# Performance work log

Measured on AMD Instinct MI355X. Metric: run time of the kernel, lower is better.

The kernel has to match this reference:

```python
import jax, jax.numpy as jnp
import numpy as np

H = 16  # heads
DH = 64  # dim_head
SCALE = DH ** -0.5


def rotate_half(x):
    x1, x2 = jnp.split(x, 2, axis=-1)
    return jnp.concatenate([-x2, x1], axis=-1)


def apply_rope(pos, t):
    # pos: [n, d] broadcast over [b, h, n, d]
    return t * jnp.cos(pos) + rotate_half(t) * jnp.sin(pos)


def setup_inputs() -> dict:
    key = jax.random.key(0)
    ks = jax.random.split(key, 6)
    B, N, D = 4, 2048, 1024
    inner = H * DH
    x = jax.random.normal(ks[0], (B, N, D), dtype=jnp.float32)
    rotary_emb = jax.random.normal(ks[1], (N, DH), dtype=jnp.float32)
    Wq = jax.random.normal(ks[2], (D, inner), dtype=jnp.float32) / np.sqrt(D)
    Wkv = jax.random.normal(ks[3], (D, 2 * inner), dtype=jnp.float32) / np.sqrt(D)
    Wout = jax.random.normal(ks[4], (inner, D), dtype=jnp.float32) / np.sqrt(inner)
    bout = jnp.zeros((D,), dtype=jnp.float32)
    return {"x": x, "rotary_emb": rotary_emb, "Wq": Wq, "Wkv": Wkv, "Wout": Wout, "bout": bout}


def reference(x, rotary_emb, Wq, Wkv, Wout, bout):
    B, N, D = x.shape
    # QKV projections (self-attention: context = x)
    q = x @ Wq                       # [b, n, h*d]
    kv = x @ Wkv                     # [b, n, 2*h*d]
    k, v = jnp.split(kv, 2, axis=-1)

    def to_heads(t):
        return t.reshape(B, N, H, DH).transpose(0, 2, 1, 3)  # [b, h, n, d]

    q, k, v = to_heads(q), to_heads(k), to_heads(v)
    q = apply_rope(rotary_emb, q)
    k = apply_rope(rotary_emb, k)

    # scaled dot-product attention
    scores = jnp.einsum('bhid,bhjd->bhij', q, k) * SCALE
    attn = jax.nn.softmax(scores, axis=-1)
    out = jnp.einsum('bhij,bhjd->bhid', attn, v)  # [b, h, n, d]
    out = out.transpose(0, 2, 1, 3).reshape(B, N, H * DH)
    return out @ Wout + bout
```

## Files before the change

### kernel.cpp

```cpp
#include <hip/hip_runtime.h>

#define BB 4
#define NN 2048
#define DD 1024
#define HH 16
#define DHH 64
#define MM (BB*NN)
#define QS 3072

typedef unsigned short u16;
typedef __attribute__((ext_vector_type(8))) short short8;
typedef __attribute__((ext_vector_type(4))) float floatx4;

#if __has_builtin(__builtin_amdgcn_exp2f)
#define EXP2F __builtin_amdgcn_exp2f
#else
#define EXP2F exp2f
#endif

__device__ __forceinline__ u16 f2bf(float f) {
  union { float f; unsigned u; } v; v.f = f;
  unsigned u = v.u;
  return (u16)((u + 0x7fffu + ((u >> 16) & 1u)) >> 16);
}
__device__ __forceinline__ float bf2f(u16 h) {
  union { unsigned u; float f; } v; v.u = ((unsigned)h) << 16;
  return v.f;
}
__device__ __forceinline__ unsigned fbits(float f) {
  union { float f; unsigned u; } v; v.f = f; return v.u;
}
__device__ __forceinline__ unsigned pkbf(float lo, float hi) {
#if __has_builtin(__builtin_amdgcn_perm)
  return __builtin_amdgcn_perm(fbits(hi), fbits(lo), 0x07060302u);
#else
  return (fbits(lo) >> 16) | (fbits(hi) & 0xffff0000u);
#endif
}
__device__ __forceinline__ void gll16(const u16* g, u16* l) {
  __builtin_amdgcn_global_load_lds((const __attribute__((address_space(1))) unsigned int*)g,
                                   (__attribute__((address_space(3))) unsigned int*)l, 16, 0, 0);
}
__device__ __forceinline__ int toff(int row, int kc) {
  int pr = row >> 1;
  int c = (((row & 1) << 2) + kc) ^ (pr & 7);
  return pr * 64 + c * 8;
}

#define SOFTMAX_SCALE 0.18033688f
#define SOFTMAX_BIAS  -28.8539008f

__global__ __launch_bounds__(256) void cvt_kernel(const float* __restrict__ in,
                                                  u16* __restrict__ out, int n) {
  int i = (blockIdx.x * 256 + threadIdx.x) * 4;
  if (i >= n) return;
  float4 v = *(const float4*)(in + i);
  u16 o[4] = {f2bf(v.x), f2bf(v.y), f2bf(v.z), f2bf(v.w)};
  *(uint2*)(out + i) = *(uint2*)o;
}

__global__ __launch_bounds__(256) void tcvt3_kernel(const float* __restrict__ Wq,
                                                    const float* __restrict__ Wkv,
                                                    const float* __restrict__ Wout,
                                                    u16* __restrict__ WT,
                                                    u16* __restrict__ WoutT) {
  __shared__ float t[64][65];
  int bx = blockIdx.x;
  const float* src;
  u16* dst;
  int C, c0;
  if (bx < 16)      { src = Wq;   dst = WT;                       C = 1024; c0 = bx * 64; }
  else if (bx < 48) { src = Wkv;  dst = WT + (size_t)DD * DD;     C = 2048; c0 = (bx - 16) * 64; }
  else              { src = Wout; dst = WoutT;                    C = 1024; c0 = (bx - 48) * 64; }
  const int R = 1024;
  int r0 = blockIdx.y * 64;
  int tid = threadIdx.x;
#pragma unroll
  for (int i = 0; i < 16; ++i) {
    int lin = i * 256 + tid;
    int rr = lin >> 6, cc = lin & 63;
    t[rr][cc] = src[(size_t)(r0 + rr) * C + c0 + cc];
  }
  __syncthreads();
#pragma unroll
  for (int i = 0; i < 16; ++i) {
    int lin = i * 256 + tid;
    int rr = lin >> 6, cc = lin & 63;
    dst[(size_t)(c0 + rr) * R + r0 + cc] = f2bf(t[cc][rr]);
  }
}

__global__ __launch_bounds__(256) void rope_tab_kernel(const float* __restrict__ rot,
                                                       float2* __restrict__ tab) {
  int i = blockIdx.x * 256 + threadIdx.x;
  float p = rot[i];
  float s, c;
  __sincosf(p, &s, &c);
  tab[i] = make_float2(c, s);
}

__global__ __launch_bounds__(256) void gemm_qkv(const u16* __restrict__ A,
                                                const u16* __restrict__ Bt,
                                                u16* __restrict__ qd,
                                                u16* __restrict__ kd,
                                                u16* __restrict__ vt,
                                                const float2* __restrict__ tab) {
  const int K = DD;
  __shared__ __align__(16) u16 lds[16384];
  int tid = threadIdx.x;
  int wave = tid >> 6, lane = tid & 63;
  int q4 = lane >> 4, l16 = lane & 15;
  int m0 = blockIdx.y * 128, n0 = blockIdx.x * 128;
  int wm = (wave >> 1) * 64, wn = (wave & 1) * 64;

  const u16* Ag = A + (size_t)m0 * K;
  const u16* Bg = Bt + (size_t)n0 * K;
  int o1 = tid, o2 = tid + 256;
  int pr1 = o1 >> 3, c1 = (o1 & 7) ^ (pr1 & 7);
  int row1 = pr1 * 2 + (c1 >> 2), kc1 = (c1 & 3) * 8;
  int pr2 = o2 >> 3, c2 = (o2 & 7) ^ (pr2 & 7);
  int row2 = pr2 * 2 + (c2 >> 2), kc2 = (c2 & 3) * 8;
  int d1 = wave * 512, d2 = 2048 + wave * 512;

  int foA[4], foB[4];
#pragma unroll
  for (int i = 0; i < 4; ++i) {
    foA[i] = toff(wm + i * 16 + l16, q4);
    foB[i] = toff(wn + i * 16 + l16, q4);
  }

  floatx4 acc[4][4];
#pragma unroll
  for (int mi = 0; mi < 4; ++mi)
#pragma unroll
    for (int ni = 0; ni < 4; ++ni) acc[mi][ni] = (floatx4){0.f, 0.f, 0.f, 0.f};

  gll16(Ag + (size_t)row1 * K + kc1, lds + d1);
  gll16(Ag + (size_t)row2 * K + kc2, lds + d2);
  gll16(Bg + (size_t)row1 * K + kc1, lds + 8192 + d1);
  gll16(Bg + (size_t)row2 * K + kc2, lds + 8192 + d2);

  for (int k0 = 0, it = 0; k0 < K; k0 += 32, ++it) {
    int boff = (it & 1) * 4096;
    if (k0 + 32 < K) {
      int nboff = 4096 - boff;
      int kn = k0 + 32;
      gll16(Ag + (size_t)row1 * K + kn + kc1, lds + nboff + d1);
      gll16(Ag + (size_t)row2 * K + kn + kc2, lds + nboff + d2);
      gll16(Bg + (size_t)row1 * K + kn + kc1, lds + 8192 + nboff + d1);
      gll16(Bg + (size_t)row2 * K + kn + kc2, lds + 8192 + nboff + d2);
      __builtin_amdgcn_s_waitcnt(0x0F74);
    } else {
      __builtin_amdgcn_s_waitcnt(0x0F70);
    }
    __builtin_amdgcn_s_barrier();
    const u16* Ac = lds + boff;
    const u16* Bc = lds + 8192 + boff;
    short8 af[4], bfr[4];
#pragma unroll
    for (int i = 0; i < 4; ++i) {
      af[i]  = *(const short8*)(Ac + foA[i]);
      bfr[i] = *(const short8*)(Bc + foB[i]);
    }
#pragma unroll
    for (int mi = 0; mi < 4; ++mi)
#pragma unroll
      for (int ni = 0; ni < 4; ++ni)
        acc[mi][ni] = __builtin_amdgcn_mfma_f32_16x16x32_bf16(af[mi], bfr[ni], acc[mi][ni], 0, 0, 0);
    __builtin_amdgcn_s_barrier();
  }

  int colbase = n0 + wn;
  int slot = colbase >> 10;
  int h = (colbase >> 6) & 15;
#pragma unroll
  for (int mi = 0; mi < 4; ++mi) {
    int mbase = m0 + wm + mi * 16 + q4 * 4;
    float vals[4][4];
    if (slot < 2) {
      float sc = slot ? 1.0f : SOFTMAX_SCALE;
#pragma unroll
      for (int r = 0; r < 4; ++r) {
        int n = (mbase + r) & (NN - 1);
#pragma unroll
        for (int ni = 0; ni < 2; ++ni) {
          int d0 = ni * 16 + l16;
          float2 cs0 = tab[n * 64 + d0];
          float2 cs1 = tab[n * 64 + d0 + 32];
          float v0 = acc[mi][ni][r], v1 = acc[mi][ni + 2][r];
          vals[ni][r]     = (v0 * cs0.x - v1 * cs0.y) * sc;
          vals[ni + 2][r] = (v1 * cs1.x + v0 * cs1.y) * sc;
        }
      }
      u16* dst = slot ? kd : qd;
#pragma unroll
      for (int ni = 0; ni < 4; ++ni)
#pragma unroll
        for (int r = 0; r < 4; ++r) {
          int m = mbase + r;
          dst[((size_t)((m >> 11) * HH + h) * NN + (m & (NN - 1))) * 64 + ni * 16 + l16] =
              f2bf(vals[ni][r]);
        }
    } else {
#pragma unroll
      for (int ni = 0; ni < 4; ++ni) {
        int d = ni * 16 + l16;
#pragma unroll
        for (int r = 0; r < 4; ++r) {
          int m = mbase + r;
          int nn = m & (NN - 1);
          vt[(size_t)((m >> 11) * HH + h) * (NN * 64) + (nn >> 6) * 4096 + d * 64 + (nn & 63)] =
              f2bf(acc[mi][ni][r]);
        }
      }
    }
  }
}

__global__ __launch_bounds__(256) void gemm_out(const u16* __restrict__ A,
                                                const u16* __restrict__ Bt,
                                                float* __restrict__ Cout,
                                                const float* __restrict__ bias,
                                                int M, int N, int K) {
  __shared__ __align__(16) u16 lds[16384];
  int tid = threadIdx.x;
  int wave = tid >> 6, lane = tid & 63;
  int q4 = lane >> 4, l16 = lane & 15;
  int m0 = blockIdx.y * 128, n0 = blockIdx.x * 128;
  int wm = (wave >> 1) * 64, wn = (wave & 1) * 64;

  const u16* Ag = A + (size_t)m0 * K;
  const u16* Bg = Bt + (size_t)n0 * K;
  int o1 = tid, o2 = tid + 256;
  int pr1 = o1 >> 3, c1 = (o1 & 7) ^ (pr1 & 7);
  int row1 = pr1 * 2 + (c1 >> 2), kc1 = (c1 & 3) * 8;
  int pr2 = o2 >> 3, c2 = (o2 & 7) ^ (pr2 & 7);
  int row2 = pr2 * 2 + (c2 >> 2), kc2 = (c2 & 3) * 8;
  int d1 = wave * 512, d2 = 2048 + wave * 512;

  int foA[4], foB[4];
#pragma unroll
  for (int i = 0; i < 4; ++i) {
    foA[i] = toff(wm + i * 16 + l16, q4);
    foB[i] = toff(wn + i * 16 + l16, q4);
  }

  floatx4 acc[4][4];
#pragma unroll
  for (int mi = 0; mi < 4; ++mi)
#pragma unroll
    for (int ni = 0; ni < 4; ++ni) acc[mi][ni] = (floatx4){0.f, 0.f, 0.f, 0.f};

  gll16(Ag + (size_t)row1 * K + kc1, lds + d1);
  gll16(Ag + (size_t)row2 * K + kc2, lds + d2);
  gll16(Bg + (size_t)row1 * K + kc1, lds + 8192 + d1);
  gll16(Bg + (size_t)row2 * K + kc2, lds + 8192 + d2);

  for (int k0 = 0, it = 0; k0 < K; k0 += 32, ++it) {
    int boff = (it & 1) * 4096;
    if (k0 + 32 < K) {
      int nboff = 4096 - boff;
      int kn = k0 + 32;
      gll16(Ag + (size_t)row1 * K + kn + kc1, lds + nboff + d1);
      gll16(Ag + (size_t)row2 * K + kn + kc2, lds + nboff + d2);
      gll16(Bg + (size_t)row1 * K + kn + kc1, lds + 8192 + nboff + d1);
      gll16(Bg + (size_t)row2 * K + kn + kc2, lds + 8192 + nboff + d2);
      __builtin_amdgcn_s_waitcnt(0x0F74);
    } else {
      __builtin_amdgcn_s_waitcnt(0x0F70);
    }
    __builtin_amdgcn_s_barrier();
    const u16* Ac = lds + boff;
    const u16* Bc = lds + 8192 + boff;
    short8 af[4], bfr[4];
#pragma unroll
    for (int i = 0; i < 4; ++i) {
      af[i]  = *(const short8*)(Ac + foA[i]);
      bfr[i] = *(const short8*)(Bc + foB[i]);
    }
#pragma unroll
    for (int mi = 0; mi < 4; ++mi)
#pragma unroll
      for (int ni = 0; ni < 4; ++ni)
        acc[mi][ni] = __builtin_amdgcn_mfma_f32_16x16x32_bf16(af[mi], bfr[ni], acc[mi][ni], 0, 0, 0);
    __builtin_amdgcn_s_barrier();
  }

#pragma unroll
  for (int ni = 0; ni < 4; ++ni) {
    int col = n0 + wn + ni * 16 + l16;
    float bval = bias[col];
#pragma unroll
    for (int mi = 0; mi < 4; ++mi) {
#pragma unroll
      for (int r = 0; r < 4; ++r) {
        int row = m0 + wm + mi * 16 + q4 * 4 + r;
        Cout[(size_t)row * N + col] = acc[mi][ni][r] + bval;
      }
    }
  }
}

__global__ __launch_bounds__(512, 4) void attn_kernel(const u16* __restrict__ qd,
                                                      const u16* __restrict__ kd,
                                                      const u16* __restrict__ vt,
                                                      u16* __restrict__ ao) {
  __shared__ __align__(16) u16 lds[16384];

  int tid = threadIdx.x, wave = tid >> 6, lane = tid & 63;
  int q4 = lane >> 4, l16 = lane & 15;
  int qt = blockIdx.x, bh = blockIdx.y, b = bh >> 4, h = bh & 15;
  const u16* qbh = qd + (size_t)bh * NN * 64;
  const u16* kbh = kd + (size_t)bh * NN * 64;
  const u16* vbh = vt + (size_t)bh * NN * 64;

  int srow = wave * 8 + (lane >> 3);
  int g = ((lane & 7) ^ ((lane >> 3) & 7)) * 8;
  int prow = ((srow >> 2) & 3) * 8 + ((srow >> 4) & 1) * 4 + (srow & 3) + ((srow >> 5) & 1) * 32;

#pragma unroll
  for (int it = 0; it < 4; ++it)
    gll16(qbh + (size_t)(qt * 256 + it * 64 + srow) * 64 + g, lds + (it * 64 + wave * 8) * 64);
  __builtin_amdgcn_s_waitcnt(0x0F70);
  __builtin_amdgcn_s_barrier();

  short8 aq[2][2];
#pragma unroll
  for (int mi = 0; mi < 2; ++mi)
#pragma unroll
    for (int ks = 0; ks < 2; ++ks) {
      int row = wave * 32 + mi * 16 + l16;
      aq[mi][ks] = *(const short8*)(lds + row * 64 + (((ks * 4 + q4) ^ (row & 7)) * 8));
    }
  __builtin_amdgcn_s_waitcnt(0xC07F);
  __builtin_amdgcn_s_barrier();

  gll16(kbh + (size_t)prow * 64 + g, lds + wave * 512);
  gll16(vbh + (size_t)srow * 64 + g, lds + 8192 + wave * 512);

  union { unsigned u[4]; short8 s8; } ones;
#pragma unroll
  for (int i = 0; i < 4; ++i) ones.u[i] = 0x3F803F80u;

  floatx4 lacc[2];
  floatx4 o[2][4];
#pragma unroll
  for (int mi = 0; mi < 2; ++mi) {
    lacc[mi] = (floatx4){0.f, 0.f, 0.f, 0.f};
#pragma unroll
    for (int di = 0; di < 4; ++di) o[mi][di] = (floatx4){0.f, 0.f, 0.f, 0.f};
  }

  for (int j0 = 0, itn = 0; j0 < NN; j0 += 64, ++itn) {
    int coff = (itn & 1) * 4096;
    if (j0 + 64 < NN) {
      int noff = 4096 - coff;
      gll16(kbh + (size_t)(j0 + 64 + prow) * 64 + g, lds + noff + wave * 512);
      gll16(vbh + (size_t)((j0 >> 6) + 1) * 4096 + srow * 64 + g, lds + 8192 + noff + wave * 512);
      __builtin_amdgcn_s_waitcnt(0x0F72);
    } else {
      __builtin_amdgcn_s_waitcnt(0x0F70);
    }
    __builtin_amdgcn_s_barrier();

    const u16* Kc = lds + coff;
    const u16* Vc = lds + 8192 + coff;

    floatx4 s[4][2];
#pragma unroll
    for (int kg = 0; kg < 4; ++kg)
#pragma unroll
      for (int mi = 0; mi < 2; ++mi)
        s[kg][mi] = (floatx4){SOFTMAX_BIAS, SOFTMAX_BIAS, SOFTMAX_BIAS, SOFTMAX_BIAS};
#pragma unroll
    for (int ks = 0; ks < 2; ++ks) {
      short8 kf[4];
#pragma unroll
      for (int kg = 0; kg < 4; ++kg) {
        int row = kg * 16 + l16;
        kf[kg] = *(const short8*)(Kc + row * 64 + (((ks * 4 + q4) ^ (row & 7)) * 8));
      }
#pragma unroll
      for (int kg = 0; kg < 4; ++kg)
#pragma unroll
        for (int mi = 0; mi < 2; ++mi)
          s[kg][mi] = __builtin_amdgcn_mfma_f32_16x16x32_bf16(kf[kg], aq[mi][ks], s[kg][mi], 0, 0, 0);
    }

    unsigned pk[4][2][2];
#pragma unroll
    for (int kg = 0; kg < 4; ++kg)
#pragma unroll
      for (int mi = 0; mi < 2; ++mi) {
        float e0 = EXP2F(s[kg][mi][0]);
        float e1 = EXP2F(s[kg][mi][1]);
        float e2 = EXP2F(s[kg][mi][2]);
        float e3 = EXP2F(s[kg][mi][3]);
        pk[kg][mi][0] = pkbf(e0, e1);
        pk[kg][mi][1] = pkbf(e2, e3);
      }

#pragma unroll
    for (int ks = 0; ks < 2; ++ks) {
      short8 vf[4];
#pragma unroll
      for (int di = 0; di < 4; ++di) {
        int row = di * 16 + l16;
        vf[di] = *(const short8*)(Vc + row * 64 + (((ks * 4 + q4) ^ (row & 7)) * 8));
      }
#pragma unroll
      for (int mi = 0; mi < 2; ++mi) {
        union { unsigned u[4]; short8 s8; } bw;
        bw.u[0] = pk[2 * ks][mi][0];
        bw.u[1] = pk[2 * ks][mi][1];
        bw.u[2] = pk[2 * ks + 1][mi][0];
        bw.u[3] = pk[2 * ks + 1][mi][1];
        lacc[mi] = __builtin_amdgcn_mfma_f32_16x16x32_bf16(ones.s8, bw.s8, lacc[mi], 0, 0, 0);
#pragma unroll
        for (int di = 0; di < 4; ++di)
          o[mi][di] = __builtin_amdgcn_mfma_f32_16x16x32_bf16(vf[di], bw.s8, o[mi][di], 0, 0, 0);
      }
    }
    __builtin_amdgcn_s_barrier();
  }

  float rinv[2];
#pragma unroll
  for (int mi = 0; mi < 2; ++mi) rinv[mi] = 1.0f / lacc[mi][0];

#pragma unroll
  for (int mi = 0; mi < 2; ++mi) {
    int qrow = qt * 256 + wave * 32 + mi * 16 + l16;
    size_t base = (size_t)(b * NN + qrow) * DD + h * DHH + q4 * 4;
#pragma unroll
    for (int di = 0; di < 4; ++di)
#pragma unroll
      for (int r = 0; r < 4; ++r)
        ao[base + di * 16 + r] = f2bf(o[mi][di][r] * rinv[mi]);
  }
}

extern "C" void kernel_launch(void* const* d_in, const int* in_sizes, int n_in,
                              void* d_out, int out_size, void* d_ws, size_t ws_size,
                              hipStream_t stream) {
  const float* x    = (const float*)d_in[0];
  const float* rot  = (const float*)d_in[1];
  const float* Wq   = (const float*)d_in[2];
  const float* Wkv  = (const float*)d_in[3];
  const float* Wout = (const float*)d_in[4];
  const float* bout = (const float*)d_in[5];
  float* out = (float*)d_out;

  char* ws = (char*)d_ws;
  size_t off = 0;
  auto alloc = [&](size_t bytes) {
    void* p = ws + off;
    off = (off + bytes + 255) & ~(size_t)255;
    return p;
  };
  u16*    xb    = (u16*)alloc((size_t)MM * DD * 2);
  u16*    WT    = (u16*)alloc((size_t)QS * DD * 2);
  u16*    WoutT = (u16*)alloc((size_t)DD * DD * 2);
  float2* tab   = (float2*)alloc((size_t)NN * DHH * 8);
  u16*    qdb   = (u16*)alloc((size_t)MM * DD * 2);
  u16*    kdb   = (u16*)alloc((size_t)MM * DD * 2);
  u16*    vtt   = (u16*)alloc((size_t)MM * DD * 2);
  u16*    ao    = (u16*)alloc((size_t)MM * DD * 2);

  cvt_kernel<<<(MM * DD / 4) / 256, 256, 0, stream>>>(x, xb, MM * DD);
  tcvt3_kernel<<<dim3(64, 16), 256, 0, stream>>>(Wq, Wkv, Wout, WT, WoutT);
  rope_tab_kernel<<<(NN * DHH) / 256, 256, 0, stream>>>(rot, tab);

  gemm_qkv<<<dim3(QS / 128, MM / 128), 256, 0, stream>>>(xb, WT, qdb, kdb, vtt, tab);

  attn_kernel<<<dim3(NN / 256, BB * HH), 512, 0, stream>>>(qdb, kdb, vtt, ao);

  gemm_out<<<dim3(DD / 128, MM / 128), 256, 0, stream>>>(ao, WoutT, out, bout, MM, DD, DD);
}
```

Measured before the change: 270.8 us.

## Restructure QKV GEMM into 256x256 tiles with staged half-tile prefetch pipeline

The QKV projection GEMM moves from 128x128 tiles on 4 waves to 256x256 tiles on 8 waves with K-steps of 64. Global-to-LDS loads are split into half-tile stages interleaved between MFMA phases, with s_setprio around the MFMA blocks. Workgroup indices are remapped so that neighbouring blocks share input tiles in cache. The aim is more data reuse per LDS byte and better overlap of loads with compute, at the cost of 128 KB of LDS and heavy register pressure from 32 accumulators, which can limit occupancy.

```diff
diff --git a/kernel.cpp b/kernel.cpp
--- a/kernel.cpp
+++ b/kernel.cpp
@@ -99,86 +99,136 @@
   tab[i] = make_float2(c, s);
 }
 
-__global__ __launch_bounds__(256) void gemm_qkv(const u16* __restrict__ A,
-                                                const u16* __restrict__ Bt,
-                                                u16* __restrict__ qd,
-                                                u16* __restrict__ kd,
-                                                u16* __restrict__ vt,
-                                                const float2* __restrict__ tab) {
+__global__ __launch_bounds__(512, 2) void gemm_qkv(const u16* __restrict__ A,
+                                                   const u16* __restrict__ Bt,
+                                                   u16* __restrict__ qd,
+                                                   u16* __restrict__ kd,
+                                                   u16* __restrict__ vt,
+                                                   const float2* __restrict__ tab) {
   const int K = DD;
-  __shared__ __align__(16) u16 lds[16384];
+  const int NT = K / 64;
+  __shared__ __align__(16) u16 lds[65536];
   int tid = threadIdx.x;
   int wave = tid >> 6, lane = tid & 63;
   int q4 = lane >> 4, l16 = lane & 15;
-  int m0 = blockIdx.y * 128, n0 = blockIdx.x * 128;
-  int wm = (wave >> 1) * 64, wn = (wave & 1) * 64;
+  int wr = wave >> 2, wc = wave & 3;
+
+  int flat = blockIdx.y * 12 + blockIdx.x;
+  int wg = (flat & 7) * 48 + (flat >> 3);
+  int bx = wg % 12, by = wg / 12;
+  int m0 = by * 256, n0 = bx * 256;
 
   const u16* Ag = A + (size_t)m0 * K;
   const u16* Bg = Bt + (size_t)n0 * K;
-  int o1 = tid, o2 = tid + 256;
-  int pr1 = o1 >> 3, c1 = (o1 & 7) ^ (pr1 & 7);
-  int row1 = pr1 * 2 + (c1 >> 2), kc1 = (c1 & 3) * 8;
-  int pr2 = o2 >> 3, c2 = (o2 & 7) ^ (pr2 & 7);
-  int row2 = pr2 * 2 + (c2 >> 2), kc2 = (c2 & 3) * 8;
-  int d1 = wave * 512, d2 = 2048 + wave * 512;
-
-  int foA[4], foB[4];
-#pragma unroll
-  for (int i = 0; i < 4; ++i) {
-    foA[i] = toff(wm + i * 16 + l16, q4);
-    foB[i] = toff(wn + i * 16 + l16, q4);
-  }
-
-  floatx4 acc[4][4];
-#pragma unroll
-  for (int mi = 0; mi < 4; ++mi)
+
+  int spr = tid >> 3, sct = tid & 7, su = sct ^ (spr & 7);
+  int srow = spr * 2 + (su >> 2);
+  int skc = (su & 3) * 8;
+  size_t so = (size_t)srow * K + skc;
+
+  int toffA[8], toffB[4];
+#pragma unroll
+  for (int mi = 0; mi < 8; ++mi) toffA[mi] = wr * 4096 + toff(mi * 16 + l16, q4);
+#pragma unroll
+  for (int ni = 0; ni < 4; ++ni)
+    toffB[ni] = (wc >> 1) * 4096 + toff((wc & 1) * 64 + ni * 16 + l16, q4);
+
+  floatx4 acc[8][4];
+#pragma unroll
+  for (int mi = 0; mi < 8; ++mi)
 #pragma unroll
     for (int ni = 0; ni < 4; ++ni) acc[mi][ni] = (floatx4){0.f, 0.f, 0.f, 0.f};
 
-  gll16(Ag + (size_t)row1 * K + kc1, lds + d1);
-  gll16(Ag + (size_t)row2 * K + kc2, lds + d2);
-  gll16(Bg + (size_t)row1 * K + kc1, lds + 8192 + d1);
-  gll16(Bg + (size_t)row2 * K + kc2, lds + 8192 + d2);
-
-  for (int k0 = 0, it = 0; k0 < K; k0 += 32, ++it) {
-    int boff = (it & 1) * 4096;
-    if (k0 + 32 < K) {
-      int nboff = 4096 - boff;
-      int kn = k0 + 32;
-      gll16(Ag + (size_t)row1 * K + kn + kc1, lds + nboff + d1);
-      gll16(Ag + (size_t)row2 * K + kn + kc2, lds + nboff + d2);
-      gll16(Bg + (size_t)row1 * K + kn + kc1, lds + 8192 + nboff + d1);
-      gll16(Bg + (size_t)row2 * K + kn + kc2, lds + 8192 + nboff + d2);
-      __builtin_amdgcn_s_waitcnt(0x0F74);
-    } else {
-      __builtin_amdgcn_s_waitcnt(0x0F70);
-    }
-    __builtin_amdgcn_s_barrier();
-    const u16* Ac = lds + boff;
-    const u16* Bc = lds + 8192 + boff;
-    short8 af[4], bfr[4];
-#pragma unroll
-    for (int i = 0; i < 4; ++i) {
-      af[i]  = *(const short8*)(Ac + foA[i]);
-      bfr[i] = *(const short8*)(Bc + foB[i]);
-    }
-#pragma unroll
-    for (int mi = 0; mi < 4; ++mi)
+  auto stageHalf = [&](int t, int mat, int kh) {
+    const u16* src = (mat ? Bg : Ag) + so + t * 64 + kh * 32;
+    u16* dst = lds + (t & 1) * 32768 + mat * 16384 + kh * 8192 + wave * 512;
+    gll16(src, dst);
+    gll16(src + (size_t)128 * K, dst + 4096);
+  };
+
+  stageHalf(0, 1, 0); stageHalf(0, 0, 0); stageHalf(0, 1, 1); stageHalf(0, 0, 1);
+  stageHalf(1, 1, 0); stageHalf(1, 0, 0); stageHalf(1, 1, 1);
+  __builtin_amdgcn_s_waitcnt(0x0F76);
+  __builtin_amdgcn_s_barrier();
+
+#pragma unroll
+  for (int t = 0; t < NT; ++t) {
+    const u16* Ab = lds + (t & 1) * 32768;
+    const u16* Bb = Ab + 16384;
+    short8 af[4], bfq[4];
+
+#pragma unroll
+    for (int ni = 0; ni < 4; ++ni) bfq[ni] = *(const short8*)(Bb + toffB[ni]);
+#pragma unroll
+    for (int f = 0; f < 4; ++f) af[f] = *(const short8*)(Ab + toffA[f]);
+    if (t + 1 < NT) stageHalf(t + 1, 0, 1);
+    __builtin_amdgcn_s_barrier();
+    __builtin_amdgcn_s_waitcnt(0xC07F);
+    __builtin_amdgcn_s_setprio(1);
+#pragma unroll
+    for (int f = 0; f < 4; ++f)
 #pragma unroll
       for (int ni = 0; ni < 4; ++ni)
-        acc[mi][ni] = __builtin_amdgcn_mfma_f32_16x16x32_bf16(af[mi], bfr[ni], acc[mi][ni], 0, 0, 0);
-    __builtin_amdgcn_s_barrier();
-  }
-
-  int colbase = n0 + wn;
+        acc[f][ni] = __builtin_amdgcn_mfma_f32_16x16x32_bf16(af[f], bfq[ni], acc[f][ni], 0, 0, 0);
+    __builtin_amdgcn_s_setprio(0);
+    __builtin_amdgcn_s_barrier();
+
+#pragma unroll
+    for (int f = 0; f < 4; ++f) af[f] = *(const short8*)(Ab + toffA[4 + f]);
+    if (t + 2 < NT) stageHalf(t + 2, 1, 0);
+    __builtin_amdgcn_s_barrier();
+    __builtin_amdgcn_s_waitcnt(0xC07F);
+    __builtin_amdgcn_s_setprio(1);
+#pragma unroll
+    for (int f = 0; f < 4; ++f)
+#pragma unroll
+      for (int ni = 0; ni < 4; ++ni)
+        acc[4 + f][ni] = __builtin_amdgcn_mfma_f32_16x16x32_bf16(af[f], bfq[ni], acc[4 + f][ni], 0, 0, 0);
+    __builtin_amdgcn_s_setprio(0);
+    __builtin_amdgcn_s_barrier();
+
+#pragma unroll
+    for (int ni = 0; ni < 4; ++ni) bfq[ni] = *(const short8*)(Bb + 8192 + toffB[ni]);
+#pragma unroll
+    for (int f = 0; f < 4; ++f) af[f] = *(const short8*)(Ab + 8192 + toffA[f]);
+    if (t + 2 < NT) stageHalf(t + 2, 0, 0);
+    __builtin_amdgcn_s_barrier();
+    __builtin_amdgcn_s_waitcnt(0xC07F);
+    __builtin_amdgcn_s_setprio(1);
+#pragma unroll
+    for (int f = 0; f < 4; ++f)
+#pragma unroll
+      for (int ni = 0; ni < 4; ++ni)
+        acc[f][ni] = __builtin_amdgcn_mfma_f32_16x16x32_bf16(af[f], bfq[ni], acc[f][ni], 0, 0, 0);
+    __builtin_amdgcn_s_setprio(0);
+    __builtin_amdgcn_s_barrier();
+
+#pragma unroll
+    for (int f = 0; f < 4; ++f) af[f] = *(const short8*)(Ab + 8192 + toffA[4 + f]);
+    if (t + 2 < NT) stageHalf(t + 2, 1, 1);
+    __builtin_amdgcn_s_barrier();
+    __builtin_amdgcn_s_waitcnt(0xC07F);
+    __builtin_amdgcn_s_setprio(1);
+#pragma unroll
+    for (int f = 0; f < 4; ++f)
+#pragma unroll
+      for (int ni = 0; ni < 4; ++ni)
+        acc[4 + f][ni] = __builtin_amdgcn_mfma_f32_16x16x32_bf16(af[f], bfq[ni], acc[4 + f][ni], 0, 0, 0);
+    __builtin_amdgcn_s_setprio(0);
+    if (t == NT - 2) __builtin_amdgcn_s_waitcnt(0x0F70);
+    else if (t < NT - 2) __builtin_amdgcn_s_waitcnt(0x0F76);
+    __builtin_amdgcn_s_barrier();
+  }
+
+  int colbase = n0 + wc * 64;
   int slot = colbase >> 10;
   int h = (colbase >> 6) & 15;
 #pragma unroll
-  for (int mi = 0; mi < 4; ++mi) {
-    int mbase = m0 + wm + mi * 16 + q4 * 4;
+  for (int mi = 0; mi < 8; ++mi) {
+    int mbase = m0 + wr * 128 + mi * 16 + q4 * 4;
     float vals[4][4];
     if (slot < 2) {
-      float sc = slot ? 1.0f : SOFTMAX_SCALE;
+      float scl = slot ? 1.0f : SOFTMAX_SCALE;
 #pragma unroll
       for (int r = 0; r < 4; ++r) {
         int n = (mbase + r) & (NN - 1);
@@ -188,8 +238,8 @@
           float2 cs0 = tab[n * 64 + d0];
           float2 cs1 = tab[n * 64 + d0 + 32];
           float v0 = acc[mi][ni][r], v1 = acc[mi][ni + 2][r];
-          vals[ni][r]     = (v0 * cs0.x - v1 * cs0.y) * sc;
-          vals[ni + 2][r] = (v1 * cs1.x + v0 * cs1.y) * sc;
+          vals[ni][r]     = (v0 * cs0.x - v1 * cs0.y) * scl;
+          vals[ni + 2][r] = (v1 * cs1.x + v0 * cs1.y) * scl;
         }
       }
       u16* dst = slot ? kd : qd;
@@ -471,7 +521,7 @@
   tcvt3_kernel<<<dim3(64, 16), 256, 0, stream>>>(Wq, Wkv, Wout, WT, WoutT);
   rope_tab_kernel<<<(NN * DHH) / 256, 256, 0, stream>>>(rot, tab);
 
-  gemm_qkv<<<dim3(QS / 128, MM / 128), 256, 0, stream>>>(xb, WT, qdb, kdb, vtt, tab);
+  gemm_qkv<<<dim3(QS / 256, MM / 256), 512, 0, stream>>>(xb, WT, qdb, kdb, vtt, tab);
 
   attn_kernel<<<dim3(NN / 256, BB * HH), 512, 0, stream>>>(qdb, kdb, vtt, ao);
 
```

Result: no change. 269.1 us (-0.6%).
